# Kernel optimization log

Measured on AMD Instinct MI355X. Metric: run time of the kernel, lower is better.

Reference implementation:

```python
import jax, jax.numpy as jnp
import numpy as np

D_IN = 1024
D_OUT = 1024
NUM_HEADS = 16
HEAD_DIM = D_OUT // NUM_HEADS


def setup_inputs() -> dict:
    key = jax.random.key(0)
    k_x, k_q, k_k, k_v, k_o, k_ob = jax.random.split(key, 6)
    s_in = 1.0 / np.sqrt(D_IN)
    s_out = 1.0 / np.sqrt(D_OUT)
    return {
        "x": jax.random.normal(k_x, (2, 2048, D_IN), dtype=jnp.float32),
        "W_q": jax.random.uniform(k_q, (D_IN, D_OUT), minval=-s_in, maxval=s_in, dtype=jnp.float32),
        "W_k": jax.random.uniform(k_k, (D_IN, D_OUT), minval=-s_in, maxval=s_in, dtype=jnp.float32),
        "W_v": jax.random.uniform(k_v, (D_IN, D_OUT), minval=-s_in, maxval=s_in, dtype=jnp.float32),
        "W_out": jax.random.uniform(k_o, (D_OUT, D_OUT), minval=-s_out, maxval=s_out, dtype=jnp.float32),
        "b_out": jax.random.uniform(k_ob, (D_OUT,), minval=-s_out, maxval=s_out, dtype=jnp.float32),
    }


def reference(x, W_q, W_k, W_v, W_out, b_out):
    b, t, _ = x.shape
    # projections (qkv_bias=False)
    q = (x @ W_q).reshape(b, t, NUM_HEADS, HEAD_DIM).transpose(0, 2, 1, 3)  # [b,h,t,d]
    k = (x @ W_k).reshape(b, t, NUM_HEADS, HEAD_DIM).transpose(0, 2, 1, 3)
    v = (x @ W_v).reshape(b, t, NUM_HEADS, HEAD_DIM).transpose(0, 2, 1, 3)
    scale = 1.0 / np.sqrt(HEAD_DIM).astype(np.float32)
    scores = jnp.einsum("bhqd,bhkd->bhqk", q, k) * scale  # [b,h,t,t]
    causal = jnp.triu(jnp.ones((t, t), dtype=bool), k=1)
    scores = jnp.where(causal, -jnp.inf, scores)
    weights = jax.nn.softmax(scores, axis=-1)
    # dropout p=0.0 -> identity
    context = jnp.einsum("bhqk,bhkd->bhqd", weights, v)
    context = context.transpose(0, 2, 1, 3).reshape(b, t, D_OUT)
    return context @ W_out + b_out
```

## Files before the change

### kernel.cpp

```cpp
#include <hip/hip_runtime.h>
#include <hip/hip_bf16.h>

#define B_  2
#define T_  2048
#define D_  1024
#define H_  16
#define DH_ 64
#define M_  (B_*T_)

typedef _Float16 f16;
typedef __attribute__((ext_vector_type(4))) _Float16 f16x4;
typedef __attribute__((ext_vector_type(8))) _Float16 f16x8;
typedef __attribute__((ext_vector_type(4))) float f32x4;

#define GLOAD_LDS(gp, lp) __builtin_amdgcn_global_load_lds( \
    (const __attribute__((address_space(1))) void*)(gp),    \
    (__attribute__((address_space(3))) void*)(lp), 16, 0, 0)

__global__ void prep(const float* __restrict__ x,
                     const float* __restrict__ wq, const float* __restrict__ wk,
                     const float* __restrict__ wv, const float* __restrict__ wo,
                     f16* __restrict__ xb, f16* __restrict__ wqkvT, f16* __restrict__ woutT) {
  __shared__ float tile[32][33];
  const int bid = blockIdx.x;
  if (bid < 2048) {
    size_t i = ((size_t)bid * 256 + threadIdx.x) * 8;
    float4 a = *(const float4*)(x + i);
    float4 b = *(const float4*)(x + i + 4);
    f16x8 o;
    o[0]=(f16)a.x; o[1]=(f16)a.y; o[2]=(f16)a.z; o[3]=(f16)a.w;
    o[4]=(f16)b.x; o[5]=(f16)b.y; o[6]=(f16)b.z; o[7]=(f16)b.w;
    *(f16x8*)(xb + i) = o;
  } else {
    const int b2 = bid - 2048;
    const int j = b2 >> 10, rem = b2 & 1023;
    const float* src = (j==0)?wq:(j==1)?wk:(j==2)?wv:wo;
    f16* dst = (j<3) ? (wqkvT + (size_t)j*D_*D_) : woutT;
    const int n0 = (rem & 31)*32, k0 = (rem >> 5)*32;
    const int tx = threadIdx.x & 31, ty = threadIdx.x >> 5;
    #pragma unroll
    for (int i=0;i<32;i+=8)
      tile[ty+i][tx] = src[(size_t)(k0+ty+i)*D_ + n0+tx];
    __syncthreads();
    #pragma unroll
    for (int i=0;i<32;i+=8)
      dst[(size_t)(n0+ty+i)*D_ + k0+tx] = (f16)tile[tx][ty+i];
  }
}

__launch_bounds__(256, 2)
__global__ void qkv_gemm(const f16* __restrict__ xb, const f16* __restrict__ wT,
                         f16* __restrict__ Qp, f16* __restrict__ Kp, f16* __restrict__ Vtp) {
  const int fid = blockIdx.x;
  const int g = fid & 7, r = fid >> 3;
  const int m0 = ((((r & 3) << 3) | g)) * 128;
  const int n0 = ((r >> 2) & 7) * 128;
  const int j  = r >> 5;
  const f16* B0 = wT + (size_t)j * D_ * D_;
  __shared__ alignas(16) char smem[65536];
  f16* AsF = (f16*)smem;
  f16* BsF = AsF + 2*128*64;
  const int tid = threadIdx.x;
  const int lane = tid & 63, wave = tid >> 6;
  const int ln = lane & 15, quad = lane >> 4;
  const int wm = wave >> 1, wn = wave & 1;

  f32x4 acc[4][4];
  #pragma unroll
  for (int a=0;a<4;++a)
    #pragma unroll
    for (int b=0;b<4;++b) acc[a][b] = f32x4{0.f,0.f,0.f,0.f};

  const bool swapped = (j < 2);
  const int slot_row[4] = { (0*256+tid)>>3, (1*256+tid)>>3, (2*256+tid)>>3, (3*256+tid)>>3 };

  #pragma unroll
  for (int p = 0; p < 4; ++p) {
    int slot = p*256 + tid;
    int row  = slot_row[p];
    int c    = (slot & 7) ^ (row & 7);
    GLOAD_LDS(xb + (size_t)(m0+row)*D_ + c*8, AsF + (size_t)slot*8);
    GLOAD_LDS(B0 + (size_t)(n0+row)*D_ + c*8, BsF + (size_t)slot*8);
  }
  __syncthreads();

  for (int it = 0; it < 16; ++it) {
    const f16* Ac = AsF + (it & 1)*8192;
    const f16* Bc = BsF + (it & 1)*8192;
    if (it < 15) {
      const int k1 = (it + 1) * 64;
      f16* An = AsF + ((it + 1) & 1)*8192;
      f16* Bn = BsF + ((it + 1) & 1)*8192;
      #pragma unroll
      for (int p = 0; p < 4; ++p) {
        int slot = p*256 + tid;
        int row  = slot_row[p];
        int c    = (slot & 7) ^ (row & 7);
        GLOAD_LDS(xb + (size_t)(m0+row)*D_ + k1 + c*8, An + (size_t)slot*8);
        GLOAD_LDS(B0 + (size_t)(n0+row)*D_ + k1 + c*8, Bn + (size_t)slot*8);
      }
    }
    #pragma unroll
    for (int ks = 0; ks < 2; ++ks) {
      const int cb = ((ks*4 + quad) ^ (ln & 7)) * 8;
      f16x8 af[4], bf[4];
      #pragma unroll
      for (int mt = 0; mt < 4; ++mt)
        af[mt] = *(const f16x8*)(Ac + (size_t)(wm*64 + mt*16 + ln)*64 + cb);
      #pragma unroll
      for (int nt = 0; nt < 4; ++nt)
        bf[nt] = *(const f16x8*)(Bc + (size_t)(wn*64 + nt*16 + ln)*64 + cb);
      if (swapped) {
        #pragma unroll
        for (int nt = 0; nt < 4; ++nt)
          #pragma unroll
          for (int mt = 0; mt < 4; ++mt)
            acc[nt][mt] = __builtin_amdgcn_mfma_f32_16x16x32_f16(bf[nt], af[mt], acc[nt][mt], 0, 0, 0);
      } else {
        #pragma unroll
        for (int mt = 0; mt < 4; ++mt)
          #pragma unroll
          for (int nt = 0; nt < 4; ++nt)
            acc[mt][nt] = __builtin_amdgcn_mfma_f32_16x16x32_f16(af[mt], bf[nt], acc[mt][nt], 0, 0, 0);
      }
    }
    __syncthreads();
  }

  if (swapped) {
    const float scale = (j == 0) ? 0.125f : 1.0f;
    f16* dstB = (j == 0) ? Qp : Kp;
    #pragma unroll
    for (int nt = 0; nt < 4; ++nt)
      #pragma unroll
      for (int mt = 0; mt < 4; ++mt) {
        int gm = m0 + wm*64 + mt*16 + ln;
        int gn = n0 + wn*64 + nt*16 + quad*4;
        int bb = gm >> 11, t = gm & (T_-1);
        int h  = gn >> 6,  dd = gn & (DH_-1);
        f16x4 v;
        #pragma unroll
        for (int rr = 0; rr < 4; ++rr) v[rr] = (f16)(acc[nt][mt][rr] * scale);
        *(f16x4*)&dstB[((((size_t)bb*H_ + h)*T_ + t)*DH_) + dd] = v;
      }
  } else {
    f16* VtS = (f16*)smem;
    #pragma unroll
    for (int mt = 0; mt < 4; ++mt)
      #pragma unroll
      for (int nt = 0; nt < 4; ++nt) {
        f16x4 v;
        v[0]=(f16)acc[mt][nt][0]; v[1]=(f16)acc[mt][nt][1];
        v[2]=(f16)acc[mt][nt][2]; v[3]=(f16)acc[mt][nt][3];
        *(f16x4*)&VtS[(size_t)(wn*64 + nt*16 + ln)*136 + wm*64 + mt*16 + quad*4] = v;
      }
    __syncthreads();
    int dd_loc = tid >> 1, half = tid & 1;
    int gn = n0 + dd_loc, h = gn >> 6, dd = gn & (DH_-1);
    int bb = m0 >> 11, tb = (m0 & (T_-1)) + half*64;
    f16* dst = Vtp + ((size_t)(bb*H_ + h)*DH_ + dd)*T_ + tb;
    const f16* src = VtS + (size_t)dd_loc*136 + half*64;
    #pragma unroll
    for (int u = 0; u < 8; ++u)
      *(uint4*)(dst + u*8) = *(const uint4*)(src + u*8);
  }
}

__launch_bounds__(256, 3)
__global__ void flash(const f16* __restrict__ Qp, const f16* __restrict__ Kp,
                      const f16* __restrict__ Vtp, f16* __restrict__ ctx) {
  const int fid = blockIdx.x;
  const int bh = fid & 31;
  const int qt = 31 - (fid >> 5);
  const int b = bh >> 4, h = bh & (H_-1);
  const f16* Kh = Kp  + (size_t)bh * T_ * DH_;
  const f16* Vh = Vtp + (size_t)bh * DH_ * T_;
  const f16* Qh = Qp  + (size_t)bh * T_ * DH_;
  const int tid = threadIdx.x, lane = tid & 63, w = tid >> 6;
  const int ln = lane & 15, quad = lane >> 4;
  __shared__ alignas(16) f16 Ks[2*64*64];
  __shared__ alignas(16) f16 Vs[2*64*64];
  __shared__ alignas(16) f16 Ps[64][72];

  const int qw = qt*64 + w*16;

  f16x8 qf[2];
  #pragma unroll
  for (int ks = 0; ks < 2; ++ks)
    qf[ks] = *(const f16x8*)&Qh[(size_t)(qw + ln)*DH_ + ks*32 + quad*8];

  f32x4 o[4];
  #pragma unroll
  for (int dt = 0; dt < 4; ++dt) o[dt] = f32x4{0.f,0.f,0.f,0.f};
  float l_part = 0.f;

  #pragma unroll
  for (int i = 0; i < 2; ++i) {
    int row = w*16 + i*8 + (lane >> 3);
    int c   = (lane & 7) ^ (row & 7);
    GLOAD_LDS(Kh + (size_t)row*DH_ + c*8, Ks + (w*128 + i*64 + lane)*8);
    GLOAD_LDS(Vh + (size_t)row*T_  + c*8, Vs + (w*128 + i*64 + lane)*8);
  }
  __syncthreads();

  for (int it = 0; it <= qt; ++it) {
    const f16* Kc = Ks + (it & 1)*4096;
    const f16* Vc = Vs + (it & 1)*4096;
    if (it < qt) {
      const int kv1 = (it + 1)*64;
      f16* Kn = Ks + ((it + 1) & 1)*4096;
      f16* Vn = Vs + ((it + 1) & 1)*4096;
      #pragma unroll
      for (int i = 0; i < 2; ++i) {
        int row = w*16 + i*8 + (lane >> 3);
        int c   = (lane & 7) ^ (row & 7);
        GLOAD_LDS(Kh + (size_t)(kv1 + row)*DH_ + c*8, Kn + (w*128 + i*64 + lane)*8);
        GLOAD_LDS(Vh + (size_t)row*T_ + kv1 + c*8,    Vn + (w*128 + i*64 + lane)*8);
      }
    }

    f32x4 s[4];
    #pragma unroll
    for (int kt = 0; kt < 4; ++kt) s[kt] = f32x4{0.f,0.f,0.f,0.f};
    #pragma unroll
    for (int ks = 0; ks < 2; ++ks) {
      f16x8 kx[4];
      #pragma unroll
      for (int kt = 0; kt < 4; ++kt)
        kx[kt] = *(const f16x8*)(Kc + (size_t)(kt*16 + ln)*64 + (((ks*4 + quad) ^ (ln & 7))*8));
      #pragma unroll
      for (int kt = 0; kt < 4; ++kt)
        s[kt] = __builtin_amdgcn_mfma_f32_16x16x32_f16(kx[kt], qf[ks], s[kt], 0, 0, 0);
    }
    if (it == qt) {
      const int kv0 = it*64;
      #pragma unroll
      for (int kt = 0; kt < 4; ++kt)
        #pragma unroll
        for (int rr = 0; rr < 4; ++rr)
          if (kv0 + kt*16 + quad*4 + rr > qw + ln) s[kt][rr] = -INFINITY;
    }
    #pragma unroll
    for (int kt = 0; kt < 4; ++kt) {
      f16x4 pk;
      #pragma unroll
      for (int rr = 0; rr < 4; ++rr) {
        float pe = __expf(s[kt][rr]);
        l_part += pe;
        pk[rr] = (f16)pe;
      }
      *(f16x4*)&Ps[w*16 + ln][kt*16 + quad*4] = pk;
    }
    asm volatile("" ::: "memory");

    #pragma unroll
    for (int ks = 0; ks < 2; ++ks) {
      f16x8 px = *(const f16x8*)&Ps[w*16 + ln][ks*32 + quad*8];
      #pragma unroll
      for (int dt = 0; dt < 4; ++dt) {
        f16x8 vy = *(const f16x8*)(Vc + (size_t)(dt*16 + ln)*64 + (((ks*4 + quad) ^ (ln & 7))*8));
        o[dt] = __builtin_amdgcn_mfma_f32_16x16x32_f16(px, vy, o[dt], 0, 0, 0);
      }
    }
    __syncthreads();
  }

  float l = l_part;
  l += __shfl_xor(l, 16, 64);
  l += __shfl_xor(l, 32, 64);
  float inv = 1.0f / l;
  #pragma unroll
  for (int rr = 0; rr < 4; ++rr) {
    float linv = __shfl(inv, quad*4 + rr, 64);
    int t = qt*64 + w*16 + quad*4 + rr;
    #pragma unroll
    for (int dt = 0; dt < 4; ++dt)
      ctx[(size_t)(b*T_ + t)*D_ + h*DH_ + dt*16 + ln] = (f16)(o[dt][rr] * linv);
  }
}

__launch_bounds__(256, 2)
__global__ void out_gemm(const f16* __restrict__ ctx, const f16* __restrict__ woT,
                         const float* __restrict__ bo, float* __restrict__ out) {
  const int fid = blockIdx.x;
  const int g = fid & 7, r = fid >> 3;
  const int m0 = ((((r & 3) << 3) | g)) * 128;
  const int n0 = (r >> 2) * 128;
  __shared__ alignas(16) f16 smem[4*128*64];
  f16* AsF = smem;
  f16* BsF = AsF + 2*128*64;
  const int tid = threadIdx.x;
  const int lane = tid & 63, wave = tid >> 6;
  const int ln = lane & 15, quad = lane >> 4;
  const int wm = wave >> 1, wn = wave & 1;

  f32x4 acc[4][4];
  #pragma unroll
  for (int a=0;a<4;++a)
    #pragma unroll
    for (int b=0;b<4;++b) acc[a][b] = f32x4{0.f,0.f,0.f,0.f};

  #pragma unroll
  for (int p = 0; p < 4; ++p) {
    int slot = p*256 + tid;
    int row  = slot >> 3;
    int c    = (slot & 7) ^ (row & 7);
    GLOAD_LDS(ctx + (size_t)(m0+row)*D_ + c*8, AsF + (size_t)slot*8);
    GLOAD_LDS(woT + (size_t)(n0+row)*D_ + c*8, BsF + (size_t)slot*8);
  }
  __syncthreads();

  for (int it = 0; it < 16; ++it) {
    const f16* Ac = AsF + (it & 1)*8192;
    const f16* Bc = BsF + (it & 1)*8192;
    if (it < 15) {
      const int k1 = (it + 1) * 64;
      f16* An = AsF + ((it + 1) & 1)*8192;
      f16* Bn = BsF + ((it + 1) & 1)*8192;
      #pragma unroll
      for (int p = 0; p < 4; ++p) {
        int slot = p*256 + tid;
        int row  = slot >> 3;
        int c    = (slot & 7) ^ (row & 7);
        GLOAD_LDS(ctx + (size_t)(m0+row)*D_ + k1 + c*8, An + (size_t)slot*8);
        GLOAD_LDS(woT + (size_t)(n0+row)*D_ + k1 + c*8, Bn + (size_t)slot*8);
      }
    }
    #pragma unroll
    for (int ks = 0; ks < 2; ++ks) {
      const int cb = ((ks*4 + quad) ^ (ln & 7)) * 8;
      f16x8 af[4], bf[4];
      #pragma unroll
      for (int mt = 0; mt < 4; ++mt)
        af[mt] = *(const f16x8*)(Ac + (size_t)(wm*64 + mt*16 + ln)*64 + cb);
      #pragma unroll
      for (int nt = 0; nt < 4; ++nt)
        bf[nt] = *(const f16x8*)(Bc + (size_t)(wn*64 + nt*16 + ln)*64 + cb);
      #pragma unroll
      for (int nt = 0; nt < 4; ++nt)
        #pragma unroll
        for (int mt = 0; mt < 4; ++mt)
          acc[nt][mt] = __builtin_amdgcn_mfma_f32_16x16x32_f16(bf[nt], af[mt], acc[nt][mt], 0, 0, 0);
    }
    __syncthreads();
  }

  #pragma unroll
  for (int nt = 0; nt < 4; ++nt) {
    int gn = n0 + wn*64 + nt*16 + quad*4;
    float4 bv = *(const float4*)&bo[gn];
    #pragma unroll
    for (int mt = 0; mt < 4; ++mt) {
      int gm = m0 + wm*64 + mt*16 + ln;
      float4 v;
      v.x = acc[nt][mt][0] + bv.x;
      v.y = acc[nt][mt][1] + bv.y;
      v.z = acc[nt][mt][2] + bv.z;
      v.w = acc[nt][mt][3] + bv.w;
      *(float4*)&out[(size_t)gm*D_ + gn] = v;
    }
  }
}

extern "C" void kernel_launch(void* const* d_in, const int* in_sizes, int n_in,
                              void* d_out, int out_size, void* d_ws, size_t ws_size,
                              hipStream_t stream) {
  const float* x  = (const float*)d_in[0];
  const float* wq = (const float*)d_in[1];
  const float* wk = (const float*)d_in[2];
  const float* wv = (const float*)d_in[3];
  const float* wo = (const float*)d_in[4];
  const float* bo = (const float*)d_in[5];
  float* out = (float*)d_out;

  f16* ws    = (f16*)d_ws;
  f16* xb    = ws;
  f16* wqkvT = xb    + (size_t)M_*D_;
  f16* woutT = wqkvT + (size_t)3*D_*D_;
  f16* Qb    = woutT + (size_t)D_*D_;
  f16* Kb    = Qb    + (size_t)M_*D_;
  f16* Vb    = Kb    + (size_t)M_*D_;
  f16* ctx   = Vb    + (size_t)M_*D_;

  prep<<<6144, 256, 0, stream>>>(x, wq, wk, wv, wo, xb, wqkvT, woutT);
  qkv_gemm<<<768, 256, 0, stream>>>(xb, wqkvT, Qb, Kb, Vb);
  flash<<<1024, 256, 0, stream>>>(Qb, Kb, Vb, ctx);
  out_gemm<<<256, 256, 0, stream>>>(ctx, woutT, bo, out);
}
```

Before: 165.3 us.

## Double query tile per flash block to reuse K/V tiles across 128 queries

Each flash attention block now handles 128 query rows (32 per wave, two 16-row groups) instead of 64, so every K/V tile loaded into LDS feeds twice as many MFMAs. The grid is halved to 512 blocks and the K/V cooperative loads are re-indexed across all threads. The aim is to cut global and LDS K/V traffic per query and amortise sync overhead. The cost is more registers and LDS per block, fewer blocks for load balance, and some wasted work on masked diagonal tiles.

```diff
diff --git a/kernel.cpp b/kernel.cpp
--- a/kernel.cpp
+++ b/kernel.cpp
@@ -171,7 +171,7 @@
                       const f16* __restrict__ Vtp, f16* __restrict__ ctx) {
   const int fid = blockIdx.x;
   const int bh = fid & 31;
-  const int qt = 31 - (fid >> 5);
+  const int qt = 15 - (fid >> 5);
   const int b = bh >> 4, h = bh & (H_-1);
   const f16* Kh = Kp  + (size_t)bh * T_ * DH_;
   const f16* Vh = Vtp + (size_t)bh * DH_ * T_;
@@ -180,48 +180,59 @@
   const int ln = lane & 15, quad = lane >> 4;
   __shared__ alignas(16) f16 Ks[2*64*64];
   __shared__ alignas(16) f16 Vs[2*64*64];
-  __shared__ alignas(16) f16 Ps[64][72];
-
-  const int qw = qt*64 + w*16;
-
-  f16x8 qf[2];
-  #pragma unroll
-  for (int ks = 0; ks < 2; ++ks)
-    qf[ks] = *(const f16x8*)&Qh[(size_t)(qw + ln)*DH_ + ks*32 + quad*8];
-
-  f32x4 o[4];
-  #pragma unroll
-  for (int dt = 0; dt < 4; ++dt) o[dt] = f32x4{0.f,0.f,0.f,0.f};
-  float l_part = 0.f;
+  __shared__ alignas(16) f16 Ps[128][72];
+
+  const int qw0 = qt*128 + w*32;
+
+  f16x8 qf[2][2];
+  #pragma unroll
+  for (int gq = 0; gq < 2; ++gq)
+    #pragma unroll
+    for (int ks = 0; ks < 2; ++ks)
+      qf[gq][ks] = *(const f16x8*)&Qh[(size_t)(qw0 + gq*16 + ln)*DH_ + ks*32 + quad*8];
+
+  f32x4 o[2][4];
+  #pragma unroll
+  for (int gq = 0; gq < 2; ++gq)
+    #pragma unroll
+    for (int dt = 0; dt < 4; ++dt) o[gq][dt] = f32x4{0.f,0.f,0.f,0.f};
+  float l_part0 = 0.f, l_part1 = 0.f;
+
+  const int it_max = 2*qt + 1;
 
   #pragma unroll
   for (int i = 0; i < 2; ++i) {
-    int row = w*16 + i*8 + (lane >> 3);
-    int c   = (lane & 7) ^ (row & 7);
-    GLOAD_LDS(Kh + (size_t)row*DH_ + c*8, Ks + (w*128 + i*64 + lane)*8);
-    GLOAD_LDS(Vh + (size_t)row*T_  + c*8, Vs + (w*128 + i*64 + lane)*8);
+    int slot = i*256 + tid;
+    int row  = slot >> 3;
+    int c    = (slot & 7) ^ (row & 7);
+    GLOAD_LDS(Kh + (size_t)row*DH_ + c*8, Ks + (size_t)slot*8);
+    GLOAD_LDS(Vh + (size_t)row*T_  + c*8, Vs + (size_t)slot*8);
   }
   __syncthreads();
 
-  for (int it = 0; it <= qt; ++it) {
+  for (int it = 0; it <= it_max; ++it) {
     const f16* Kc = Ks + (it & 1)*4096;
     const f16* Vc = Vs + (it & 1)*4096;
-    if (it < qt) {
+    if (it < it_max) {
       const int kv1 = (it + 1)*64;
       f16* Kn = Ks + ((it + 1) & 1)*4096;
       f16* Vn = Vs + ((it + 1) & 1)*4096;
       #pragma unroll
       for (int i = 0; i < 2; ++i) {
-        int row = w*16 + i*8 + (lane >> 3);
-        int c   = (lane & 7) ^ (row & 7);
-        GLOAD_LDS(Kh + (size_t)(kv1 + row)*DH_ + c*8, Kn + (w*128 + i*64 + lane)*8);
-        GLOAD_LDS(Vh + (size_t)row*T_ + kv1 + c*8,    Vn + (w*128 + i*64 + lane)*8);
-      }
-    }
-
-    f32x4 s[4];
-    #pragma unroll
-    for (int kt = 0; kt < 4; ++kt) s[kt] = f32x4{0.f,0.f,0.f,0.f};
+        int slot = i*256 + tid;
+        int row  = slot >> 3;
+        int c    = (slot & 7) ^ (row & 7);
+        GLOAD_LDS(Kh + (size_t)(kv1 + row)*DH_ + c*8, Kn + (size_t)slot*8);
+        GLOAD_LDS(Vh + (size_t)row*T_ + kv1 + c*8,    Vn + (size_t)slot*8);
+      }
+    }
+    const int kv0 = it*64;
+
+    f32x4 s[2][4];
+    #pragma unroll
+    for (int gq = 0; gq < 2; ++gq)
+      #pragma unroll
+      for (int kt = 0; kt < 4; ++kt) s[gq][kt] = f32x4{0.f,0.f,0.f,0.f};
     #pragma unroll
     for (int ks = 0; ks < 2; ++ks) {
       f16x8 kx[4];
@@ -229,53 +240,64 @@
       for (int kt = 0; kt < 4; ++kt)
         kx[kt] = *(const f16x8*)(Kc + (size_t)(kt*16 + ln)*64 + (((ks*4 + quad) ^ (ln & 7))*8));
       #pragma unroll
-      for (int kt = 0; kt < 4; ++kt)
-        s[kt] = __builtin_amdgcn_mfma_f32_16x16x32_f16(kx[kt], qf[ks], s[kt], 0, 0, 0);
-    }
-    if (it == qt) {
-      const int kv0 = it*64;
-      #pragma unroll
-      for (int kt = 0; kt < 4; ++kt)
-        #pragma unroll
-        for (int rr = 0; rr < 4; ++rr)
-          if (kv0 + kt*16 + quad*4 + rr > qw + ln) s[kt][rr] = -INFINITY;
-    }
-    #pragma unroll
-    for (int kt = 0; kt < 4; ++kt) {
-      f16x4 pk;
-      #pragma unroll
-      for (int rr = 0; rr < 4; ++rr) {
-        float pe = __expf(s[kt][rr]);
-        l_part += pe;
-        pk[rr] = (f16)pe;
-      }
-      *(f16x4*)&Ps[w*16 + ln][kt*16 + quad*4] = pk;
+      for (int kt = 0; kt < 4; ++kt) {
+        s[0][kt] = __builtin_amdgcn_mfma_f32_16x16x32_f16(kx[kt], qf[0][ks], s[0][kt], 0, 0, 0);
+        s[1][kt] = __builtin_amdgcn_mfma_f32_16x16x32_f16(kx[kt], qf[1][ks], s[1][kt], 0, 0, 0);
+      }
+    }
+
+    #pragma unroll
+    for (int gq = 0; gq < 2; ++gq) {
+      const int qwg = qw0 + gq*16;
+      if (kv0 + 63 > qwg) {
+        #pragma unroll
+        for (int kt = 0; kt < 4; ++kt)
+          #pragma unroll
+          for (int rr = 0; rr < 4; ++rr)
+            if (kv0 + kt*16 + quad*4 + rr > qwg + ln) s[gq][kt][rr] = -INFINITY;
+      }
+      #pragma unroll
+      for (int kt = 0; kt < 4; ++kt) {
+        f16x4 pk;
+        #pragma unroll
+        for (int rr = 0; rr < 4; ++rr) {
+          float pe = __expf(s[gq][kt][rr]);
+          if (gq == 0) l_part0 += pe; else l_part1 += pe;
+          pk[rr] = (f16)pe;
+        }
+        *(f16x4*)&Ps[w*32 + gq*16 + ln][kt*16 + quad*4] = pk;
+      }
     }
     asm volatile("" ::: "memory");
 
     #pragma unroll
     for (int ks = 0; ks < 2; ++ks) {
-      f16x8 px = *(const f16x8*)&Ps[w*16 + ln][ks*32 + quad*8];
+      f16x8 px0 = *(const f16x8*)&Ps[w*32 + ln][ks*32 + quad*8];
+      f16x8 px1 = *(const f16x8*)&Ps[w*32 + 16 + ln][ks*32 + quad*8];
       #pragma unroll
       for (int dt = 0; dt < 4; ++dt) {
         f16x8 vy = *(const f16x8*)(Vc + (size_t)(dt*16 + ln)*64 + (((ks*4 + quad) ^ (ln & 7))*8));
-        o[dt] = __builtin_amdgcn_mfma_f32_16x16x32_f16(px, vy, o[dt], 0, 0, 0);
+        o[0][dt] = __builtin_amdgcn_mfma_f32_16x16x32_f16(px0, vy, o[0][dt], 0, 0, 0);
+        o[1][dt] = __builtin_amdgcn_mfma_f32_16x16x32_f16(px1, vy, o[1][dt], 0, 0, 0);
       }
     }
     __syncthreads();
   }
 
-  float l = l_part;
-  l += __shfl_xor(l, 16, 64);
-  l += __shfl_xor(l, 32, 64);
-  float inv = 1.0f / l;
-  #pragma unroll
-  for (int rr = 0; rr < 4; ++rr) {
-    float linv = __shfl(inv, quad*4 + rr, 64);
-    int t = qt*64 + w*16 + quad*4 + rr;
-    #pragma unroll
-    for (int dt = 0; dt < 4; ++dt)
-      ctx[(size_t)(b*T_ + t)*D_ + h*DH_ + dt*16 + ln] = (f16)(o[dt][rr] * linv);
+  #pragma unroll
+  for (int gq = 0; gq < 2; ++gq) {
+    float l = (gq == 0) ? l_part0 : l_part1;
+    l += __shfl_xor(l, 16, 64);
+    l += __shfl_xor(l, 32, 64);
+    float inv = 1.0f / l;
+    #pragma unroll
+    for (int rr = 0; rr < 4; ++rr) {
+      float linv = __shfl(inv, quad*4 + rr, 64);
+      int t = qt*128 + w*32 + gq*16 + quad*4 + rr;
+      #pragma unroll
+      for (int dt = 0; dt < 4; ++dt)
+        ctx[(size_t)(b*T_ + t)*D_ + h*DH_ + dt*16 + ln] = (f16)(o[gq][dt][rr] * linv);
+    }
   }
 }
 
@@ -384,6 +406,6 @@
 
   prep<<<6144, 256, 0, stream>>>(x, wq, wk, wv, wo, xb, wqkvT, woutT);
   qkv_gemm<<<768, 256, 0, stream>>>(xb, wqkvT, Qb, Kb, Vb);
-  flash<<<1024, 256, 0, stream>>>(Qb, Kb, Vb, ctx);
+  flash<<<512, 256, 0, stream>>>(Qb, Kb, Vb, ctx);
   out_gemm<<<256, 256, 0, stream>>>(ctx, woutT, bo, out);
 }
```

After: 179.5 us. 8.6% more time.

## Split flash attention KV across waves and reduce partial outputs in LDS

Applied to the files above, without the earlier changes.

The flash kernel now has each wave own 16 key rows of every 64-key tile for all 64 queries, instead of 16 queries against all keys. This removes the P round trip through shared memory: the probabilities stay in registers and feed a 16x16x16 MFMA directly. Partial O and row sums are combined across waves through a serialized LDS reduction at the end, followed by vectorized stores. Q is prescaled by log2(e) so exp2 replaces expf. The cost is four times more O accumulator registers per wave and an extra reduction phase with several barriers.

```diff
diff --git a/kernel.cpp b/kernel.cpp
--- a/kernel.cpp
+++ b/kernel.cpp
@@ -128,7 +128,7 @@
   }
 
   if (swapped) {
-    const float scale = (j == 0) ? 0.125f : 1.0f;
+    const float scale = (j == 0) ? (0.125f * 1.44269504088896f) : 1.0f;
     f16* dstB = (j == 0) ? Qp : Kp;
     #pragma unroll
     for (int nt = 0; nt < 4; ++nt)
@@ -178,28 +178,32 @@
   const f16* Qh = Qp  + (size_t)bh * T_ * DH_;
   const int tid = threadIdx.x, lane = tid & 63, w = tid >> 6;
   const int ln = lane & 15, quad = lane >> 4;
-  __shared__ alignas(16) f16 Ks[2*64*64];
-  __shared__ alignas(16) f16 Vs[2*64*64];
-  __shared__ alignas(16) f16 Ps[64][72];
-
-  const int qw = qt*64 + w*16;
-
-  f16x8 qf[2];
-  #pragma unroll
-  for (int ks = 0; ks < 2; ++ks)
-    qf[ks] = *(const f16x8*)&Qh[(size_t)(qw + ln)*DH_ + ks*32 + quad*8];
-
-  f32x4 o[4];
-  #pragma unroll
-  for (int dt = 0; dt < 4; ++dt) o[dt] = f32x4{0.f,0.f,0.f,0.f};
-  float l_part = 0.f;
+
+  __shared__ alignas(16) char smem[32768];
+  f16* Ks = (f16*)smem;
+  f16* Vs = (f16*)(smem + 16384);
+
+  f16x8 qf[4][2];
+  #pragma unroll
+  for (int g = 0; g < 4; ++g)
+    #pragma unroll
+    for (int ks = 0; ks < 2; ++ks)
+      qf[g][ks] = *(const f16x8*)&Qh[(size_t)(qt*64 + g*16 + ln)*DH_ + ks*32 + quad*8];
+
+  f32x4 o[4][4];
+  #pragma unroll
+  for (int dt = 0; dt < 4; ++dt)
+    #pragma unroll
+    for (int g = 0; g < 4; ++g) o[dt][g] = f32x4{0.f,0.f,0.f,0.f};
+  float lp[4] = {0.f, 0.f, 0.f, 0.f};
 
   #pragma unroll
   for (int i = 0; i < 2; ++i) {
-    int row = w*16 + i*8 + (lane >> 3);
-    int c   = (lane & 7) ^ (row & 7);
-    GLOAD_LDS(Kh + (size_t)row*DH_ + c*8, Ks + (w*128 + i*64 + lane)*8);
-    GLOAD_LDS(Vh + (size_t)row*T_  + c*8, Vs + (w*128 + i*64 + lane)*8);
+    int slot = i*256 + tid;
+    int row  = slot >> 3;
+    int c    = (slot & 7) ^ (row & 7);
+    GLOAD_LDS(Kh + (size_t)row*DH_ + c*8, Ks + (size_t)slot*8);
+    GLOAD_LDS(Vh + (size_t)row*T_  + c*8, Vs + (size_t)slot*8);
   }
   __syncthreads();
 
@@ -212,71 +216,118 @@
       f16* Vn = Vs + ((it + 1) & 1)*4096;
       #pragma unroll
       for (int i = 0; i < 2; ++i) {
-        int row = w*16 + i*8 + (lane >> 3);
-        int c   = (lane & 7) ^ (row & 7);
-        GLOAD_LDS(Kh + (size_t)(kv1 + row)*DH_ + c*8, Kn + (w*128 + i*64 + lane)*8);
-        GLOAD_LDS(Vh + (size_t)row*T_ + kv1 + c*8,    Vn + (w*128 + i*64 + lane)*8);
+        int slot = i*256 + tid;
+        int row  = slot >> 3;
+        int c    = (slot & 7) ^ (row & 7);
+        GLOAD_LDS(Kh + (size_t)(kv1 + row)*DH_ + c*8, Kn + (size_t)slot*8);
+        GLOAD_LDS(Vh + (size_t)row*T_ + kv1 + c*8,    Vn + (size_t)slot*8);
       }
     }
 
     f32x4 s[4];
     #pragma unroll
-    for (int kt = 0; kt < 4; ++kt) s[kt] = f32x4{0.f,0.f,0.f,0.f};
+    for (int g = 0; g < 4; ++g) s[g] = f32x4{0.f,0.f,0.f,0.f};
     #pragma unroll
     for (int ks = 0; ks < 2; ++ks) {
-      f16x8 kx[4];
-      #pragma unroll
-      for (int kt = 0; kt < 4; ++kt)
-        kx[kt] = *(const f16x8*)(Kc + (size_t)(kt*16 + ln)*64 + (((ks*4 + quad) ^ (ln & 7))*8));
-      #pragma unroll
-      for (int kt = 0; kt < 4; ++kt)
-        s[kt] = __builtin_amdgcn_mfma_f32_16x16x32_f16(kx[kt], qf[ks], s[kt], 0, 0, 0);
-    }
+      f16x8 kx = *(const f16x8*)(Kc + (size_t)(w*16 + ln)*64 + (((ks*4 + quad) ^ (ln & 7))*8));
+      #pragma unroll
+      for (int g = 0; g < 4; ++g)
+        s[g] = __builtin_amdgcn_mfma_f32_16x16x32_f16(kx, qf[g][ks], s[g], 0, 0, 0);
+    }
+
     if (it == qt) {
-      const int kv0 = it*64;
-      #pragma unroll
-      for (int kt = 0; kt < 4; ++kt)
+      #pragma unroll
+      for (int g = 0; g < 4; ++g)
         #pragma unroll
         for (int rr = 0; rr < 4; ++rr)
-          if (kv0 + kt*16 + quad*4 + rr > qw + ln) s[kt][rr] = -INFINITY;
-    }
-    #pragma unroll
-    for (int kt = 0; kt < 4; ++kt) {
-      f16x4 pk;
+          if (w*16 + quad*4 + rr > g*16 + ln) s[g][rr] = -INFINITY;
+    }
+
+    f16x4 pb[4];
+    #pragma unroll
+    for (int g = 0; g < 4; ++g) {
       #pragma unroll
       for (int rr = 0; rr < 4; ++rr) {
-        float pe = __expf(s[kt][rr]);
-        l_part += pe;
-        pk[rr] = (f16)pe;
-      }
-      *(f16x4*)&Ps[w*16 + ln][kt*16 + quad*4] = pk;
-    }
-    asm volatile("" ::: "memory");
-
-    #pragma unroll
-    for (int ks = 0; ks < 2; ++ks) {
-      f16x8 px = *(const f16x8*)&Ps[w*16 + ln][ks*32 + quad*8];
-      #pragma unroll
-      for (int dt = 0; dt < 4; ++dt) {
-        f16x8 vy = *(const f16x8*)(Vc + (size_t)(dt*16 + ln)*64 + (((ks*4 + quad) ^ (ln & 7))*8));
-        o[dt] = __builtin_amdgcn_mfma_f32_16x16x32_f16(px, vy, o[dt], 0, 0, 0);
-      }
+        float pe = __builtin_amdgcn_exp2f(s[g][rr]);
+        lp[g] += pe;
+        pb[g][rr] = (f16)pe;
+      }
+    }
+
+    #pragma unroll
+    for (int dt = 0; dt < 4; ++dt) {
+      f16x4 vf = *(const f16x4*)(Vc + (size_t)(dt*16 + ln)*64
+                   + (((2*w + (quad >> 1)) ^ (ln & 7))*8) + (quad & 1)*4);
+      #pragma unroll
+      for (int g = 0; g < 4; ++g)
+        o[dt][g] = __builtin_amdgcn_mfma_f32_16x16x16f16(vf, pb[g], o[dt][g], 0, 0, 0);
     }
     __syncthreads();
   }
 
-  float l = l_part;
-  l += __shfl_xor(l, 16, 64);
-  l += __shfl_xor(l, 32, 64);
-  float inv = 1.0f / l;
-  #pragma unroll
-  for (int rr = 0; rr < 4; ++rr) {
-    float linv = __shfl(inv, quad*4 + rr, 64);
-    int t = qt*64 + w*16 + quad*4 + rr;
-    #pragma unroll
-    for (int dt = 0; dt < 4; ++dt)
-      ctx[(size_t)(b*T_ + t)*D_ + h*DH_ + dt*16 + ln] = (f16)(o[dt][rr] * linv);
-  }
+  #pragma unroll
+  for (int g = 0; g < 4; ++g) {
+    lp[g] += __shfl_xor(lp[g], 16, 64);
+    lp[g] += __shfl_xor(lp[g], 32, 64);
+  }
+
+  float* buf = (float*)smem;
+  #define WR_PART() do {                                                        \
+    _Pragma("unroll")                                                           \
+    for (int dt = 0; dt < 4; ++dt)                                              \
+      _Pragma("unroll")                                                         \
+      for (int g = 0; g < 4; ++g)                                               \
+        *(f32x4*)&buf[(size_t)(g*16 + ln)*68 + dt*16 + quad*4] = o[dt][g];      \
+    if (quad == 0) {                                                            \
+      _Pragma("unroll")                                                         \
+      for (int g = 0; g < 4; ++g) buf[64*68 + g*16 + ln] = lp[g];               \
+    }                                                                           \
+  } while (0)
+  #define ACC_PART() do {                                                       \
+    _Pragma("unroll")                                                           \
+    for (int dt = 0; dt < 4; ++dt)                                              \
+      _Pragma("unroll")                                                         \
+      for (int g = 0; g < 4; ++g) {                                             \
+        f32x4 v = *(const f32x4*)&buf[(size_t)(g*16 + ln)*68 + dt*16 + quad*4]; \
+        o[dt][g][0] += v[0]; o[dt][g][1] += v[1];                               \
+        o[dt][g][2] += v[2]; o[dt][g][3] += v[3];                               \
+      }                                                                         \
+    _Pragma("unroll")                                                           \
+    for (int g = 0; g < 4; ++g) lp[g] += buf[64*68 + g*16 + ln];                \
+  } while (0)
+
+  if (w == 1) WR_PART();
+  __syncthreads();
+  if (w == 0) ACC_PART();
+  __syncthreads();
+  if (w == 2) WR_PART();
+  __syncthreads();
+  if (w == 0) ACC_PART();
+  __syncthreads();
+  if (w == 3) WR_PART();
+  __syncthreads();
+  if (w == 0) ACC_PART();
+  __syncthreads();
+  if (w == 0) WR_PART();
+  __syncthreads();
+
+  {
+    const int q  = tid >> 2;
+    const int dc = (tid & 3) << 4;
+    const float linv = 1.0f / buf[64*68 + q];
+    const float* src = &buf[(size_t)q*68 + dc];
+    f16x8 o0, o1;
+    #pragma unroll
+    for (int jj = 0; jj < 8; ++jj) {
+      o0[jj] = (f16)(src[jj] * linv);
+      o1[jj] = (f16)(src[8 + jj] * linv);
+    }
+    f16* dst = &ctx[(size_t)(b*T_ + qt*64 + q)*D_ + h*DH_ + dc];
+    *(f16x8*)dst       = o0;
+    *(f16x8*)(dst + 8) = o1;
+  }
+  #undef WR_PART
+  #undef ACC_PART
 }
 
 __launch_bounds__(256, 2)
```

Measured after the change: 167.5 us (median of 2 runs). About the same (+1.3%).
